# Optimization experiments

Measured on AMD Instinct MI355X. Metric: run time of the kernel, lower is better.

## Reference

```python
import jax, jax.numpy as jnp
import numpy as np

B, S, D, H, DK, DV = 4, 2048, 1024, 16, 64, 64
LN_EPS = 1e-5

def setup_inputs() -> dict:
    key = jax.random.key(0)
    ks = jax.random.split(key, 5)
    s = 0.02  # init scale for weights
    return {
        "tokens": jax.random.normal(ks[0], (B, S, D), jnp.float32),
        "Wq": jax.random.normal(ks[1], (H, D, DK), jnp.float32) * s,
        "Wk": jax.random.normal(ks[2], (H, D, DK), jnp.float32) * s,
        "Wv": jax.random.normal(ks[3], (H, D, DV), jnp.float32) * s,
        "Wo": jax.random.normal(ks[4], (H * DV, D), jnp.float32) * s,
        "gamma": jnp.ones((D,), jnp.float32),
        "beta": jnp.zeros((D,), jnp.float32),
    }

def reference(tokens, Wq, Wk, Wv, Wo, gamma, beta):
    # tokens: [B,S,D]; Wq/Wk: [H,D,DK]; Wv: [H,D,DV]; Wo: [H*DV, D]
    d_k = Wq.shape[-1]
    q = jnp.einsum('bsd,hdk->bhsk', tokens, Wq)
    k = jnp.einsum('bsd,hdk->bhsk', tokens, Wk)
    v = jnp.einsum('bsd,hdv->bhsv', tokens, Wv)
    # Faithful quirk of the original: attention() returns (Q K^T / sqrt(d_k)).transpose,
    # so attn[b,h,j,i] = q_i . k_j / sqrt(d_k) and softmax runs over the QUERY index i.
    attn = jnp.einsum('bhik,bhjk->bhji', q, k) / jnp.sqrt(jnp.float32(d_k))
    attn = jax.nn.softmax(attn, axis=-1)
    heads = jnp.einsum('bhji,bhiv->bhjv', attn, v)          # [B,H,S,DV]
    b, s = tokens.shape[0], tokens.shape[1]
    multi = jnp.transpose(heads, (0, 2, 1, 3)).reshape(b, s, -1)  # concat heads
    out = multi @ Wo + tokens                                # out-proj + residual
    mu = jnp.mean(out, axis=-1, keepdims=True)
    var = jnp.var(out, axis=-1, keepdims=True)
    out = (out - mu) / jnp.sqrt(var + LN_EPS) * gamma + beta  # LayerNorm
    return out
```

## Files before the change

kernel.cpp:

```cpp
#include <hip/hip_runtime.h>
#include <hip/hip_bf16.h>
#include <stdint.h>

typedef __attribute__((ext_vector_type(4))) float f32x4;
typedef __attribute__((ext_vector_type(16))) float f32x16;
typedef __attribute__((ext_vector_type(8))) short bf16x8;
typedef __attribute__((ext_vector_type(4))) unsigned short u16x4;
typedef unsigned short u16;
typedef uint32_t u32;

#define B_ 4
#define S_ 2048
#define D_ 1024
#define H_ 16
#define DK_ 64
#define BS_ (B_*S_)
#define NQKV_ (3*H_*DK_)
#define NT_ (S_/64)

#define QSCALE 0.18033688011112042f

__device__ __forceinline__ u16 f2bf(float x) {
  union { float f; uint32_t u; } c; c.f = x;
  uint32_t r = (c.u + 0x7FFFu + ((c.u >> 16) & 1u)) >> 16;
  return (u16)r;
}

__device__ __forceinline__ float exp2_fast(float x) {
  float r; asm("v_exp_f32 %0, %1" : "=v"(r) : "v"(x)); return r;
}

__device__ __forceinline__ void gl_lds16(const u16* g, u16* l) {
  __builtin_amdgcn_global_load_lds(
      (const __attribute__((address_space(1))) u32*)g,
      (__attribute__((address_space(3))) u32*)l, 16, 0, 0);
}

__global__ __launch_bounds__(256) void conv_f32_to_bf16(
    const float* __restrict__ src, u16* __restrict__ dst, int n) {
  int i = (blockIdx.x * 256 + threadIdx.x) * 4;
  if (i >= n) return;
  const float* p = src + i;
  u16x4 o = { f2bf(p[0]), f2bf(p[1]), f2bf(p[2]), f2bf(p[3]) };
  *(u16x4*)(dst + i) = o;
}

__global__ __launch_bounds__(256) void build_wcatT(
    const float* __restrict__ Wq, const float* __restrict__ Wk,
    const float* __restrict__ Wv, u16* __restrict__ dst) {
  __shared__ float Tl[64][65];
  const int slice = blockIdx.y;
  const int w = slice >> 4, hh = slice & 15;
  const int d0 = blockIdx.x * 64;
  const float scale = (w == 0) ? QSCALE : 1.0f;
  const float* src = (w == 0 ? Wq : (w == 1 ? Wk : Wv)) + (long)hh * D_ * DK_;
  {
    int r = threadIdx.x >> 2, c = (threadIdx.x & 3) * 16;
    const float* g = src + (long)(d0 + r) * DK_ + c;
#pragma unroll
    for (int j = 0; j < 16; ++j) Tl[r][c + j] = g[j];
  }
  __syncthreads();
  {
    int dk = threadIdx.x >> 2, c = (threadIdx.x & 3) * 16;
    __attribute__((aligned(16))) u16 tmp[16];
#pragma unroll
    for (int j = 0; j < 16; ++j) tmp[j] = f2bf(Tl[c + j][dk] * scale);
    u16* o = dst + ((long)slice * 64 + dk) * D_ + d0 + c;
    *(bf16x8*)o = *(const bf16x8*)&tmp[0];
    *(bf16x8*)(o + 8) = *(const bf16x8*)&tmp[8];
  }
}

__global__ __launch_bounds__(256) void transpose_f2b(
    const float* __restrict__ src, u16* __restrict__ dst, int R, int C) {
  __shared__ float Tl[64][65];
  const int r0 = blockIdx.y * 64, c0 = blockIdx.x * 64;
  {
    int r = threadIdx.x >> 2, c = (threadIdx.x & 3) * 16;
    const float* g = src + (long)(r0 + r) * C + c0 + c;
#pragma unroll
    for (int j = 0; j < 16; ++j) Tl[r][c + j] = g[j];
  }
  __syncthreads();
  {
    int rr = threadIdx.x >> 2, c = (threadIdx.x & 3) * 16;
    __attribute__((aligned(16))) u16 tmp[16];
#pragma unroll
    for (int j = 0; j < 16; ++j) tmp[j] = f2bf(Tl[c + j][rr]);
    u16* o = dst + (long)(c0 + rr) * R + r0 + c;
    *(bf16x8*)o = *(const bf16x8*)&tmp[0];
    *(bf16x8*)(o + 8) = *(const bf16x8*)&tmp[8];
  }
}

template<bool OUT_BF16>
__global__ __launch_bounds__(256) void gemm_bf16(
    const u16* __restrict__ A, const u16* __restrict__ BT,
    void* __restrict__ Cout, const float* __restrict__ resid,
    int M, int N, int K) {
  __shared__ __attribute__((aligned(16))) u16 Al[128][32];
  __shared__ __attribute__((aligned(16))) u16 Bl[128][32];
  const int tid = threadIdx.x;
  const int wid = tid >> 6;
  const int lane = tid & 63;
  const int wm = (wid >> 1) * 64;
  const int wn = (wid & 1) * 64;
  const int row0 = blockIdx.x * 128;
  const int col0 = blockIdx.y * 128;
  const int fr = lane & 15;
  const int g = lane >> 4;

  const int srow = lane >> 2;
  const int sch = lane & 3;

  f32x4 acc[4][4] = {};

  for (int kk = 0; kk < K; kk += 32) {
    __syncthreads();
#pragma unroll
    for (int s = 0; s < 2; ++s) {
      int r = 32 * wid + 16 * s + srow;
      int gc = (sch ^ ((r >> 1) & 3)) * 8;
      gl_lds16(A + (long)(row0 + r) * K + kk + gc, &Al[32 * wid + 16 * s][0]);
      gl_lds16(BT + (long)(col0 + r) * K + kk + gc, &Bl[32 * wid + 16 * s][0]);
    }
    __syncthreads();
    bf16x8 af[4], bfr[4];
#pragma unroll
    for (int mf = 0; mf < 4; ++mf) {
      int row = wm + mf * 16 + fr;
      af[mf] = *(const bf16x8*)&Al[row][(g ^ ((row >> 1) & 3)) * 8];
    }
#pragma unroll
    for (int nf = 0; nf < 4; ++nf) {
      int row = wn + nf * 16 + fr;
      bfr[nf] = *(const bf16x8*)&Bl[row][(g ^ ((row >> 1) & 3)) * 8];
    }
    __builtin_amdgcn_s_setprio(1);
#pragma unroll
    for (int mf = 0; mf < 4; ++mf)
#pragma unroll
      for (int nf = 0; nf < 4; ++nf)
        acc[mf][nf] = __builtin_amdgcn_mfma_f32_16x16x32_bf16(
            af[mf], bfr[nf], acc[mf][nf], 0, 0, 0);
    __builtin_amdgcn_s_setprio(0);
  }

  const int r0 = (lane >> 4) * 4;
#pragma unroll
  for (int mf = 0; mf < 4; ++mf)
#pragma unroll
    for (int nf = 0; nf < 4; ++nf)
#pragma unroll
      for (int r = 0; r < 4; ++r) {
        long row = row0 + wm + mf * 16 + r0 + r;
        long col = col0 + wn + nf * 16 + fr;
        if constexpr (OUT_BF16) {
          ((u16*)Cout)[row * N + col] = f2bf(acc[mf][nf][r]);
        } else {
          float v = acc[mf][nf][r] + resid[row * N + col];
          ((float*)Cout)[row * N + col] = v;
        }
      }
}

__global__ __launch_bounds__(256) void vtrans_kernel(
    const u16* __restrict__ qkv, u16* __restrict__ vt) {
  __shared__ __attribute__((aligned(16))) u16 Tl[64][72];
  const int tid = threadIdx.x;
  const int bh = blockIdx.y, b = bh >> 4, hh = bh & 15;
  const long i0 = (long)blockIdx.x * 64;
  const int cbV = (2 * H_ + hh) * 64;
  {
    int r = tid >> 2, c = (tid & 3) * 16;
    const u16* g = qkv + ((long)b * S_ + i0 + r) * NQKV_ + cbV + c;
    *(bf16x8*)&Tl[r][c] = *(const bf16x8*)g;
    *(bf16x8*)&Tl[r][c + 8] = *(const bf16x8*)(g + 8);
  }
  __syncthreads();
  {
    int d = tid >> 2, c = (tid & 3) * 16;
    __attribute__((aligned(16))) u16 tmp[16];
#pragma unroll
    for (int j = 0; j < 16; ++j) tmp[j] = Tl[c + j][d];
    u16* o = vt + ((long)bh * 64 + d) * S_ + i0 + c;
    *(bf16x8*)o = *(const bf16x8*)&tmp[0];
    *(bf16x8*)(o + 8) = *(const bf16x8*)&tmp[8];
  }
}

__global__ __launch_bounds__(512, 4) void attn_kernel(
    const u16* __restrict__ qkv, const u16* __restrict__ vt,
    u16* __restrict__ multi) {
  __shared__ __attribute__((aligned(16))) u16 smem[3][2][64][64];
  const int tid = threadIdx.x;
  const int wid = tid >> 6;
  const int lane = tid & 63;
  const int jl = lane & 31;
  const int h = lane >> 5;

  const int bh = blockIdx.y;
  const int b = bh >> 4, hh = bh & 15;
  const long rowb = (long)b * S_;
  const long rj0 = rowb + (long)blockIdx.x * 256 + wid * 32;
  const int cbQ = hh * 64, cbK = (H_ + hh) * 64;

#define XF(r) (((r) ^ ((r) >> 3)) & 7)

  bf16x8 kf[4];
  const u16* kbase = qkv + (rj0 + jl) * NQKV_ + cbK + 8 * h;
#pragma unroll
  for (int ks = 0; ks < 4; ++ks) kf[ks] = *(const bf16x8*)(kbase + 16 * ks);

  const int strow = 8 * wid + (lane >> 3);
  const int stoff = ((lane & 7) ^ XF(strow)) * 8;
  const u16* qsrc = qkv + (rowb + strow) * NQKV_ + cbQ + stoff;
  const u16* vsrc = vt + ((long)bh * 64 + strow) * S_ + stoff;

  f32x16 accT[2] = {};
  float l_run = 0.f;

  auto compute = [&](int cur) {
    f32x16 st[2] = {};
    __builtin_amdgcn_s_setprio(1);
#pragma unroll
    for (int mb = 0; mb < 2; ++mb) {
      int row = 32 * mb + jl;
#pragma unroll
      for (int ks = 0; ks < 4; ++ks) {
        bf16x8 qf = *(const bf16x8*)&smem[cur][0][row][((2 * ks + h) ^ XF(row)) * 8];
        st[mb] = __builtin_amdgcn_mfma_f32_32x32x16_bf16(qf, kf[ks], st[mb], 0, 0, 0);
      }
    }
    __builtin_amdgcn_s_setprio(0);

    float lsum = 0.f;
#pragma unroll
    for (int mb = 0; mb < 2; ++mb)
#pragma unroll
      for (int r = 0; r < 16; ++r) {
        float pv = exp2_fast(st[mb][r]);
        st[mb][r] = pv;
        lsum += pv;
      }
    lsum += __shfl_xor(lsum, 32);
    l_run += lsum;

    uint32_t q32[2][8];
#pragma unroll
    for (int mb = 0; mb < 2; ++mb)
#pragma unroll
      for (int rp = 0; rp < 8; ++rp) {
        __hip_bfloat162 bb = __float22bfloat162_rn(
            make_float2(st[mb][2 * rp], st[mb][2 * rp + 1]));
        uint32_t w; __builtin_memcpy(&w, &bb, 4);
        q32[mb][rp] = w;
      }

    __builtin_amdgcn_s_setprio(1);
#pragma unroll
    for (int ks = 0; ks < 4; ++ks) {
      const int mb = ks >> 1;
      const int A0 = (2 * ks) & 3, A1 = (2 * ks + 1) & 3;
      uint32_t a0 = q32[mb][2 * A0], a1 = q32[mb][2 * A1];
      uint32_t b0 = q32[mb][2 * A0 + 1], b1 = q32[mb][2 * A1 + 1];
      asm("v_permlane32_swap_b32 %0, %1" : "+v"(a0), "+v"(a1));
      asm("v_permlane32_swap_b32 %0, %1" : "+v"(b0), "+v"(b1));
      union { bf16x8 v; uint32_t u[4]; } pa;
      pa.u[0] = a0; pa.u[1] = b0; pa.u[2] = a1; pa.u[3] = b1;
#pragma unroll
      for (int mb2 = 0; mb2 < 2; ++mb2) {
        int row = 32 * mb2 + jl;
        bf16x8 vf = *(const bf16x8*)&smem[cur][1][row][((2 * ks + h) ^ XF(row)) * 8];
        accT[mb2] = __builtin_amdgcn_mfma_f32_32x32x16_bf16(vf, pa.v, accT[mb2], 0, 0, 0);
      }
    }
    __builtin_amdgcn_s_setprio(0);
  };

  gl_lds16(qsrc, &smem[0][0][8 * wid][0]);
  gl_lds16(vsrc, &smem[0][1][8 * wid][0]);
  qsrc += (long)64 * NQKV_; vsrc += 64;

  for (int it = 0; it < NT_ - 1; ++it) {
    const int nx = (it + 1) % 3;
    gl_lds16(qsrc, &smem[nx][0][8 * wid][0]);
    gl_lds16(vsrc, &smem[nx][1][8 * wid][0]);
    qsrc += (long)64 * NQKV_; vsrc += 64;
    asm volatile("s_waitcnt vmcnt(2)" ::: "memory");
    __builtin_amdgcn_s_barrier();
    compute(it % 3);
  }
  asm volatile("s_waitcnt vmcnt(0)" ::: "memory");
  __builtin_amdgcn_s_barrier();
  compute((NT_ - 1) % 3);
#undef XF

  __syncthreads();
  u16 (*Wl)[32][72] = (u16 (*)[32][72])&smem[0][0][0][0];
  float inv = 1.f / l_run;
#pragma unroll
  for (int mb2 = 0; mb2 < 2; ++mb2)
#pragma unroll
    for (int r = 0; r < 16; ++r) {
      int d = 32 * mb2 + (r & 3) + 8 * (r >> 2) + 4 * h;
      Wl[wid][jl][d] = f2bf(accT[mb2][r] * inv);
    }
  int j2 = lane >> 1, dh = (lane & 1) * 32;
#pragma unroll
  for (int c = 0; c < 4; ++c) {
    bf16x8 vrow = *(const bf16x8*)&Wl[wid][j2][dh + 8 * c];
    *(bf16x8*)(multi + (rj0 + j2) * (H_ * DK_) + hh * 64 + dh + 8 * c) = vrow;
  }
}

__global__ __launch_bounds__(256) void ln_kernel(
    float* __restrict__ out, const float* __restrict__ gamma,
    const float* __restrict__ beta) {
  const int tid = threadIdx.x;
  const int wid = tid >> 6;
  const int lane = tid & 63;
  float* p = out + (long)blockIdx.x * D_;
  const float* pv = p + tid * 4;
  float x0 = pv[0], x1 = pv[1], x2 = pv[2], x3 = pv[3];
  float s = x0 + x1 + x2 + x3;
  float q = x0 * x0 + x1 * x1 + x2 * x2 + x3 * x3;
#pragma unroll
  for (int off = 32; off > 0; off >>= 1) {
    s += __shfl_down(s, off);
    q += __shfl_down(q, off);
  }
  __shared__ float sh[8];
  if (lane == 0) { sh[wid] = s; sh[4 + wid] = q; }
  __syncthreads();
  s = sh[0] + sh[1] + sh[2] + sh[3];
  q = sh[4] + sh[5] + sh[6] + sh[7];
  float mean = s * (1.0f / D_);
  float var = q * (1.0f / D_) - mean * mean;
  float rstd = rsqrtf(var + 1e-5f);
  const float* g = gamma + tid * 4;
  const float* be = beta + tid * 4;
  float* po = p + tid * 4;
  po[0] = (x0 - mean) * rstd * g[0] + be[0];
  po[1] = (x1 - mean) * rstd * g[1] + be[1];
  po[2] = (x2 - mean) * rstd * g[2] + be[2];
  po[3] = (x3 - mean) * rstd * g[3] + be[3];
}

extern "C" void kernel_launch(void* const* d_in, const int* in_sizes, int n_in,
                              void* d_out, int out_size, void* d_ws, size_t ws_size,
                              hipStream_t stream) {
  const float* tokens = (const float*)d_in[0];
  const float* Wq = (const float*)d_in[1];
  const float* Wk = (const float*)d_in[2];
  const float* Wv = (const float*)d_in[3];
  const float* Wo = (const float*)d_in[4];
  const float* gamma = (const float*)d_in[5];
  const float* beta = (const float*)d_in[6];
  float* out = (float*)d_out;

  char* ws = (char*)d_ws;
  u16* tok_bf = (u16*)(ws);
  u16* wcatT  = (u16*)(ws + 16777216);
  u16* woT    = (u16*)(ws + 23068672);
  u16* qkv    = (u16*)(ws + 25165824);
  u16* multi  = (u16*)(ws + 75497472);
  u16* vt     = (u16*)(ws + 92274688);

  conv_f32_to_bf16<<<8192, 256, 0, stream>>>(tokens, tok_bf, BS_ * D_);
  build_wcatT<<<dim3(16, 48), 256, 0, stream>>>(Wq, Wk, Wv, wcatT);
  transpose_f2b<<<dim3(16, 16), 256, 0, stream>>>(Wo, woT, D_, D_);

  gemm_bf16<true><<<dim3(BS_ / 128, NQKV_ / 128), 256, 0, stream>>>(
      tok_bf, wcatT, qkv, nullptr, BS_, NQKV_, D_);

  vtrans_kernel<<<dim3(S_ / 64, B_ * H_), 256, 0, stream>>>(qkv, vt);

  attn_kernel<<<dim3(S_ / 256, B_ * H_), 512, 0, stream>>>(qkv, vt, multi);

  gemm_bf16<false><<<dim3(BS_ / 128, D_ / 128), 256, 0, stream>>>(
      multi, woT, out, tokens, BS_, D_, D_);

  ln_kernel<<<BS_, 256, 0, stream>>>(out, gamma, beta);
}
```

Measured before the change: 209.4 us.

## Triple-buffer GEMM, fuse V transpose into QKV epilogue, remap attention grid

The GEMM now uses a three-stage LDS ring with a single barrier per K step and waitcnt-based prefetch, replacing the two-syncthreads loop. The QKV GEMM epilogue writes V tiles directly in transposed layout, so the separate vtrans kernel and its extra read/write pass go away. The attention kernel uses a 1D grid with head-major block ordering, and its softmax row sum is split into four independent accumulators to shorten the dependency chain. In exchange, the GEMM uses three times the shared memory, which may lower occupancy, and the transposed V stores are narrow scattered 8-byte writes.

```diff
diff --git a/kernel.cpp b/kernel.cpp
--- a/kernel.cpp
+++ b/kernel.cpp
@@ -94,13 +94,13 @@
   }
 }
 
-template<bool OUT_BF16>
+template<bool OUT_BF16, bool VSPLIT>
 __global__ __launch_bounds__(256) void gemm_bf16(
     const u16* __restrict__ A, const u16* __restrict__ BT,
     void* __restrict__ Cout, const float* __restrict__ resid,
-    int M, int N, int K) {
-  __shared__ __attribute__((aligned(16))) u16 Al[128][32];
-  __shared__ __attribute__((aligned(16))) u16 Bl[128][32];
+    u16* __restrict__ vtout, int M, int N, int K) {
+  __shared__ __attribute__((aligned(16))) u16 Al[3][128][32];
+  __shared__ __attribute__((aligned(16))) u16 Bl[3][128][32];
   const int tid = threadIdx.x;
   const int wid = tid >> 6;
   const int lane = tid & 63;
@@ -114,28 +114,44 @@
   const int srow = lane >> 2;
   const int sch = lane & 3;
 
+  const int r0a = 32 * wid + srow;
   f32x4 acc[4][4] = {};
 
-  for (int kk = 0; kk < K; kk += 32) {
-    __syncthreads();
-#pragma unroll
-    for (int s = 0; s < 2; ++s) {
-      int r = 32 * wid + 16 * s + srow;
-      int gc = (sch ^ ((r >> 1) & 3)) * 8;
-      gl_lds16(A + (long)(row0 + r) * K + kk + gc, &Al[32 * wid + 16 * s][0]);
-      gl_lds16(BT + (long)(col0 + r) * K + kk + gc, &Bl[32 * wid + 16 * s][0]);
-    }
-    __syncthreads();
+#define GSTAGE(bufi, kk)                                                       \
+  {                                                                            \
+    _Pragma("unroll")                                                          \
+    for (int s = 0; s < 2; ++s) {                                              \
+      int r = r0a + 16 * s;                                                    \
+      int gc = (sch ^ ((r >> 1) & 3)) * 8;                                     \
+      gl_lds16(A + (long)(row0 + r) * K + (kk) + gc, &Al[bufi][32 * wid + 16 * s][0]); \
+      gl_lds16(BT + (long)(col0 + r) * K + (kk) + gc, &Bl[bufi][32 * wid + 16 * s][0]); \
+    }                                                                          \
+  }
+
+  const int nt = K >> 5;
+  GSTAGE(0, 0);
+
+  for (int t = 0; t < nt; ++t) {
+    const int cur = t % 3;
+    if (t + 1 < nt) {
+      GSTAGE((t + 1) % 3, (t + 1) << 5);
+      asm volatile("s_waitcnt vmcnt(4)" ::: "memory");
+    } else {
+      asm volatile("s_waitcnt vmcnt(0)" ::: "memory");
+    }
+    __builtin_amdgcn_s_barrier();
+    asm volatile("" ::: "memory");
+
     bf16x8 af[4], bfr[4];
 #pragma unroll
     for (int mf = 0; mf < 4; ++mf) {
       int row = wm + mf * 16 + fr;
-      af[mf] = *(const bf16x8*)&Al[row][(g ^ ((row >> 1) & 3)) * 8];
+      af[mf] = *(const bf16x8*)&Al[cur][row][(g ^ ((row >> 1) & 3)) * 8];
     }
 #pragma unroll
     for (int nf = 0; nf < 4; ++nf) {
       int row = wn + nf * 16 + fr;
-      bfr[nf] = *(const bf16x8*)&Bl[row][(g ^ ((row >> 1) & 3)) * 8];
+      bfr[nf] = *(const bf16x8*)&Bl[cur][row][(g ^ ((row >> 1) & 3)) * 8];
     }
     __builtin_amdgcn_s_setprio(1);
 #pragma unroll
@@ -146,8 +162,26 @@
             af[mf], bfr[nf], acc[mf][nf], 0, 0, 0);
     __builtin_amdgcn_s_setprio(0);
   }
+#undef GSTAGE
 
   const int r0 = (lane >> 4) * 4;
+  if constexpr (VSPLIT) {
+    if (col0 >= 2048) {
+#pragma unroll
+      for (int mf = 0; mf < 4; ++mf)
+#pragma unroll
+        for (int nf = 0; nf < 4; ++nf) {
+          int colv = col0 + wn + nf * 16 + fr - 2048;
+          long row = row0 + wm + mf * 16 + r0;
+          int b2 = (int)(row >> 11);
+          int i = (int)(row & 2047);
+          u16x4 o = { f2bf(acc[mf][nf][0]), f2bf(acc[mf][nf][1]),
+                      f2bf(acc[mf][nf][2]), f2bf(acc[mf][nf][3]) };
+          *(u16x4*)(vtout + ((long)(b2 * 16 + (colv >> 6)) * 64 + (colv & 63)) * S_ + i) = o;
+        }
+      return;
+    }
+  }
 #pragma unroll
   for (int mf = 0; mf < 4; ++mf)
 #pragma unroll
@@ -165,31 +199,6 @@
       }
 }
 
-__global__ __launch_bounds__(256) void vtrans_kernel(
-    const u16* __restrict__ qkv, u16* __restrict__ vt) {
-  __shared__ __attribute__((aligned(16))) u16 Tl[64][72];
-  const int tid = threadIdx.x;
-  const int bh = blockIdx.y, b = bh >> 4, hh = bh & 15;
-  const long i0 = (long)blockIdx.x * 64;
-  const int cbV = (2 * H_ + hh) * 64;
-  {
-    int r = tid >> 2, c = (tid & 3) * 16;
-    const u16* g = qkv + ((long)b * S_ + i0 + r) * NQKV_ + cbV + c;
-    *(bf16x8*)&Tl[r][c] = *(const bf16x8*)g;
-    *(bf16x8*)&Tl[r][c + 8] = *(const bf16x8*)(g + 8);
-  }
-  __syncthreads();
-  {
-    int d = tid >> 2, c = (tid & 3) * 16;
-    __attribute__((aligned(16))) u16 tmp[16];
-#pragma unroll
-    for (int j = 0; j < 16; ++j) tmp[j] = Tl[c + j][d];
-    u16* o = vt + ((long)bh * 64 + d) * S_ + i0 + c;
-    *(bf16x8*)o = *(const bf16x8*)&tmp[0];
-    *(bf16x8*)(o + 8) = *(const bf16x8*)&tmp[8];
-  }
-}
-
 __global__ __launch_bounds__(512, 4) void attn_kernel(
     const u16* __restrict__ qkv, const u16* __restrict__ vt,
     u16* __restrict__ multi) {
@@ -200,10 +209,12 @@
   const int jl = lane & 31;
   const int h = lane >> 5;
 
-  const int bh = blockIdx.y;
+  const int bid = blockIdx.x;
+  const int bh = bid & 63;
+  const int jt = bid >> 6;
   const int b = bh >> 4, hh = bh & 15;
   const long rowb = (long)b * S_;
-  const long rj0 = rowb + (long)blockIdx.x * 256 + wid * 32;
+  const long rj0 = rowb + (long)jt * 256 + wid * 32;
   const int cbQ = hh * 64, cbK = (H_ + hh) * 64;
 
 #define XF(r) (((r) ^ ((r) >> 3)) & 7)
@@ -235,15 +246,20 @@
     }
     __builtin_amdgcn_s_setprio(0);
 
-    float lsum = 0.f;
+    float ls0 = 0.f, ls1 = 0.f, ls2 = 0.f, ls3 = 0.f;
 #pragma unroll
     for (int mb = 0; mb < 2; ++mb)
 #pragma unroll
-      for (int r = 0; r < 16; ++r) {
-        float pv = exp2_fast(st[mb][r]);
-        st[mb][r] = pv;
-        lsum += pv;
+      for (int r = 0; r < 16; r += 4) {
+        float p0 = exp2_fast(st[mb][r + 0]);
+        float p1 = exp2_fast(st[mb][r + 1]);
+        float p2 = exp2_fast(st[mb][r + 2]);
+        float p3 = exp2_fast(st[mb][r + 3]);
+        st[mb][r + 0] = p0; st[mb][r + 1] = p1;
+        st[mb][r + 2] = p2; st[mb][r + 3] = p3;
+        ls0 += p0; ls1 += p1; ls2 += p2; ls3 += p3;
       }
+    float lsum = (ls0 + ls1) + (ls2 + ls3);
     lsum += __shfl_xor(lsum, 32);
     l_run += lsum;
 
@@ -290,10 +306,12 @@
     qsrc += (long)64 * NQKV_; vsrc += 64;
     asm volatile("s_waitcnt vmcnt(2)" ::: "memory");
     __builtin_amdgcn_s_barrier();
+    asm volatile("" ::: "memory");
     compute(it % 3);
   }
   asm volatile("s_waitcnt vmcnt(0)" ::: "memory");
   __builtin_amdgcn_s_barrier();
+  asm volatile("" ::: "memory");
   compute((NT_ - 1) % 3);
 #undef XF
 
@@ -372,15 +390,13 @@
   build_wcatT<<<dim3(16, 48), 256, 0, stream>>>(Wq, Wk, Wv, wcatT);
   transpose_f2b<<<dim3(16, 16), 256, 0, stream>>>(Wo, woT, D_, D_);
 
-  gemm_bf16<true><<<dim3(BS_ / 128, NQKV_ / 128), 256, 0, stream>>>(
-      tok_bf, wcatT, qkv, nullptr, BS_, NQKV_, D_);
-
-  vtrans_kernel<<<dim3(S_ / 64, B_ * H_), 256, 0, stream>>>(qkv, vt);
-
-  attn_kernel<<<dim3(S_ / 256, B_ * H_), 512, 0, stream>>>(qkv, vt, multi);
-
-  gemm_bf16<false><<<dim3(BS_ / 128, D_ / 128), 256, 0, stream>>>(
-      multi, woT, out, tokens, BS_, D_, D_);
+  gemm_bf16<true, true><<<dim3(BS_ / 128, NQKV_ / 128), 256, 0, stream>>>(
+      tok_bf, wcatT, qkv, nullptr, vt, BS_, NQKV_, D_);
+
+  attn_kernel<<<512, 512, 0, stream>>>(qkv, vt, multi);
+
+  gemm_bf16<false, false><<<dim3(BS_ / 128, D_ / 128), 256, 0, stream>>>(
+      multi, woT, out, tokens, nullptr, BS_, D_, D_);
 
   ln_kernel<<<BS_, 256, 0, stream>>>(out, gamma, beta);
 }
```

Result: faster. 198.0 us (-5.4%).
